# Performance work log

Measured on AMD Instinct MI355X. Metric: run time of the kernel, lower is better.

Reference implementation:

```python
import jax, jax.numpy as jnp
import numpy as np

D_MODEL, NUM_HEADS, D_HEAD, N_CTX = 768, 12, 64, 2048
BATCH = 2


def setup_inputs() -> dict:
    key = jax.random.key(0)
    kx, kk, kq, kv, ko = jax.random.split(key, 5)
    s = 1.0 / np.sqrt(D_MODEL).astype(np.float32)
    x = jax.random.normal(kx, (BATCH, N_CTX, D_MODEL), dtype=jnp.float32)
    W_K = jax.random.normal(kk, (NUM_HEADS, D_HEAD, D_MODEL), dtype=jnp.float32) * s
    W_Q = jax.random.normal(kq, (NUM_HEADS, D_HEAD, D_MODEL), dtype=jnp.float32) * s
    W_V = jax.random.normal(kv, (NUM_HEADS, D_HEAD, D_MODEL), dtype=jnp.float32) * s
    W_O = jax.random.normal(ko, (D_MODEL, D_HEAD * NUM_HEADS), dtype=jnp.float32) * s
    return {"x": x, "W_K": W_K, "W_Q": W_Q, "W_V": W_V, "W_O": W_O}


def reference(x, W_K, W_Q, W_V, W_O):
    B, P, _ = x.shape
    d_head = W_K.shape[1]
    # per-head projections: [B, H, P, d_head]
    q = jnp.einsum('hed,bpd->bhpe', W_Q, x)
    k = jnp.einsum('hed,bpd->bhpe', W_K, x)
    v = jnp.einsum('hed,bpd->bhpe', W_V, x)
    # causal scores [B, H, Q, K]
    scores = jnp.einsum('bhqe,bhke->bhqk', q, k) / np.sqrt(d_head).astype(np.float32)
    mask = jnp.tril(jnp.ones((P, P), dtype=bool))
    scores = jnp.where(mask, scores, jnp.asarray(-1e9, scores.dtype))
    attn = jax.nn.softmax(scores, axis=-1)
    z = jnp.einsum('bhqk,bhke->bhqe', attn, v)
    # flatten heads head-major: 'b h q e -> b q (h e)'
    z_flat = z.transpose(0, 2, 1, 3).reshape(B, P, -1)
    return jnp.einsum('bpf,df->bpd', z_flat, W_O)
```

## Files before the change

kernel.cpp:

```cpp
#include <hip/hip_runtime.h>
#include <hip/hip_bf16.h>

typedef __attribute__((ext_vector_type(8))) short bf16x8;
typedef __attribute__((ext_vector_type(4))) float f32x4;
typedef __attribute__((ext_vector_type(16))) float f32x16;

static __device__ __forceinline__ unsigned short f2bf(float f) {
  union { float f; unsigned int u; } v; v.f = f;
  unsigned int u = v.u;
  return (unsigned short)((u + 0x7FFFu + ((u >> 16) & 1u)) >> 16);
}

__device__ __forceinline__ void async_ld16(const void* g, void* l) {
  __builtin_amdgcn_global_load_lds(
      (const __attribute__((address_space(1))) unsigned int*)g,
      (__attribute__((address_space(3))) unsigned int*)l, 16, 0, 0);
}

__global__ __launch_bounds__(256) void cvt_all(
    const float* __restrict__ x, const float* __restrict__ wk,
    const float* __restrict__ wq, const float* __restrict__ wv,
    const float* __restrict__ wo,
    unsigned short* __restrict__ x_bf, unsigned short* __restrict__ wkqv4,
    unsigned short* __restrict__ wo4) {
  int i = blockIdx.x * 256 + threadIdx.x;
  int e0 = i * 4;
  if (e0 < 3145728) {
    float4 v = *(const float4*)(x + e0);
    ushort4 r;
    r.x = f2bf(v.x); r.y = f2bf(v.y); r.z = f2bf(v.z); r.w = f2bf(v.w);
    *(ushort4*)(x_bf + e0) = r;
    return;
  }
  int j = e0 - 3145728;
  int a = j / 589824;
  int off = j - a * 589824;
  int nl = off / 768;
  int k = off - nl * 768;
  const float* src;
  unsigned short* dst;
  int m;
  float scale = 1.0f;
  if (a == 0)      { src = wk; m = nl;        dst = wkqv4; }
  else if (a == 1) { src = wq; m = 768 + nl;  dst = wkqv4; scale = 0.18033688011112042f; }
  else if (a == 2) { src = wv; m = 1536 + nl; dst = wkqv4; }
  else             { src = wo; m = nl;        dst = wo4; }
  float4 v = *(const float4*)(src + off);
  long idx = ((long)(m >> 4) * 24 + (k >> 5)) * 512 + (m & 15) * 32 + (k & 31);
  ushort4 r;
  r.x = f2bf(v.x * scale); r.y = f2bf(v.y * scale);
  r.z = f2bf(v.z * scale); r.w = f2bf(v.w * scale);
  *(ushort4*)(dst + idx) = r;
}

template <int MODE>
__device__ __forceinline__ void gemm_body(
    const unsigned short* __restrict__ A,
    const unsigned short* __restrict__ B4,
    void* __restrict__ outK, void* __restrict__ outQ, void* __restrict__ outV,
    int m0, int n0,
    unsigned short (*As)[8192]) {
  const int tid = threadIdx.x;
  const int w = tid >> 6;
  const int l = tid & 63;
  const int g = l >> 4;
  const int c = l & 15;
  const int wr = w >> 1, wc = w & 1;

  f32x4 acc[4][3];
#pragma unroll
  for (int i = 0; i < 4; i++)
#pragma unroll
    for (int j = 0; j < 3; j++) acc[i][j] = (f32x4){0.f, 0.f, 0.f, 0.f};

  const int lrow = l >> 3;
  const int lcolx = ((l & 7) ^ lrow) * 8;
  const unsigned short* pB = B4 + (long)((n0 >> 4) + wc * 3) * 12288 + c * 32 + g * 8;

  auto stageA = [&](int buf, int kt) {
    const int k0 = kt * 64;
#pragma unroll
    for (int cc = 0; cc < 4; ++cc) {
      int chunk = cc * 4 + w;
      int row = chunk * 8 + lrow;
      async_ld16(A + (long)(m0 + row) * 768 + k0 + lcolx, &As[buf][chunk * 512]);
    }
  };
  auto loadB = [&](bf16x8 (*b)[3], int kt) {
#pragma unroll
    for (int ks = 0; ks < 2; ++ks)
#pragma unroll
      for (int ni = 0; ni < 3; ++ni)
        b[ks][ni] = *(const bf16x8*)(pB + (long)ni * 12288 + (kt * 2 + ks) * 512);
  };
  auto step = [&](const bf16x8* asrc, const bf16x8 (*b)[3]) {
  };

  bf16x8 b0[2][3], b1[2][3];
  stageA(0, 0);
  loadB(b0, 0);

#pragma unroll
  for (int kt = 0; kt < 12; kt += 2) {
    if (kt + 1 < 12) loadB(b1, kt + 1);
    __builtin_amdgcn_sched_barrier(0);
    asm volatile("s_waitcnt vmcnt(6)" ::: "memory");
    __builtin_amdgcn_sched_barrier(0);
    __builtin_amdgcn_s_barrier();
    __builtin_amdgcn_sched_barrier(0);
    if (kt + 1 < 12) stageA(1, kt + 1);
#pragma unroll
    for (int ks = 0; ks < 2; ++ks) {
      bf16x8 a[4];
#pragma unroll
      for (int mi = 0; mi < 4; ++mi) {
        int row = wr * 64 + mi * 16 + c;
        int col = (ks * 32 + g * 8) ^ ((row & 7) * 8);
        a[mi] = *(const bf16x8*)&As[0][row * 64 + col];
      }
#pragma unroll
      for (int mi = 0; mi < 4; ++mi)
#pragma unroll
        for (int ni = 0; ni < 3; ++ni)
          acc[mi][ni] = __builtin_amdgcn_mfma_f32_16x16x32_bf16(a[mi], b0[ks][ni], acc[mi][ni], 0, 0, 0);
    }
    if (kt + 2 < 12) loadB(b0, kt + 2);
    __builtin_amdgcn_sched_barrier(0);
    if (kt + 2 < 12) {
      asm volatile("s_waitcnt vmcnt(6)" ::: "memory");
    } else {
      asm volatile("s_waitcnt vmcnt(0)" ::: "memory");
    }
    __builtin_amdgcn_sched_barrier(0);
    __builtin_amdgcn_s_barrier();
    __builtin_amdgcn_sched_barrier(0);
    if (kt + 2 < 12) stageA(0, kt + 2);
#pragma unroll
    for (int ks = 0; ks < 2; ++ks) {
      bf16x8 a[4];
#pragma unroll
      for (int mi = 0; mi < 4; ++mi) {
        int row = wr * 64 + mi * 16 + c;
        int col = (ks * 32 + g * 8) ^ ((row & 7) * 8);
        a[mi] = *(const bf16x8*)&As[1][row * 64 + col];
      }
#pragma unroll
      for (int mi = 0; mi < 4; ++mi)
#pragma unroll
        for (int ni = 0; ni < 3; ++ni)
          acc[mi][ni] = __builtin_amdgcn_mfma_f32_16x16x32_bf16(a[mi], b1[ks][ni], acc[mi][ni], 0, 0, 0);
    }
  }

  if (MODE == 1) {
    float* O = (float*)outK;
#pragma unroll
    for (int mi = 0; mi < 4; ++mi)
#pragma unroll
      for (int ni = 0; ni < 3; ++ni)
#pragma unroll
        for (int r = 0; r < 4; ++r) {
          int m = m0 + wr * 64 + mi * 16 + g * 4 + r;
          int n = n0 + wc * 48 + ni * 16 + c;
          O[(long)m * 768 + n] = acc[mi][ni][r];
        }
  } else {
    const int which = (n0 >= 1536) ? 2 : (n0 >= 768 ? 1 : 0);
    const int nb = n0 - which * 768;
    const int b = m0 >> 11;
    if (which == 2) {
#pragma unroll
      for (int mi = 0; mi < 4; ++mi)
#pragma unroll
        for (int ni = 0; ni < 3; ++ni) {
          int e = nb + wc * 48 + ni * 16 + c;
          int h = e >> 6, el = e & 63;
          long bh = b * 12 + h;
          int p0 = (m0 & 2047) + wr * 64 + mi * 16 + g * 4;
          long idx = bh * 131072 + (p0 >> 4) * 1024 + el * 16 + (p0 & 15);
          ushort4 pk;
          pk.x = f2bf(acc[mi][ni][0]); pk.y = f2bf(acc[mi][ni][1]);
          pk.z = f2bf(acc[mi][ni][2]); pk.w = f2bf(acc[mi][ni][3]);
          *(ushort4*)&((unsigned short*)outV)[idx] = pk;
        }
    } else {
#pragma unroll
      for (int mi = 0; mi < 4; ++mi)
#pragma unroll
        for (int ni = 0; ni < 3; ++ni)
#pragma unroll
          for (int r = 0; r < 4; ++r) {
            int m = m0 + wr * 64 + mi * 16 + g * 4 + r;
            int nn = nb + wc * 48 + ni * 16 + c;
            int p = m & 2047;
            int h = nn >> 6, e = nn & 63;
            unsigned short val = f2bf(acc[mi][ni][r]);
            long bh = b * 12 + h;
            if (which == 0) {
              long idx = bh * 131072 + (p >> 5) * 2048 + (e >> 4) * 512 + (p & 31) * 16 + (e & 15);
              ((unsigned short*)outK)[idx] = val;
            } else {
              ((unsigned short*)outQ)[((bh * 2048 + p) << 6) + e] = val;
            }
          }
    }
  }
}

__global__ __launch_bounds__(256) void gemm_qkv(
    const unsigned short* __restrict__ A,
    const unsigned short* __restrict__ Wkqv4,
    unsigned short* __restrict__ k4b, unsigned short* __restrict__ qb,
    unsigned short* __restrict__ v4b) {
  __shared__ __align__(16) unsigned short As[2][8192];
  const int lb = blockIdx.x;
  const int xcd = lb & 7, idx = lb >> 3;
  const int mg = xcd >> 1, ng = xcd & 1;
  const int mi = idx / 12, ni = idx - 12 * mi;
  gemm_body<0>(A, Wkqv4, k4b, qb, v4b, (mg * 8 + mi) * 128, (ng * 12 + ni) * 96, As);
}

__global__ __launch_bounds__(256) void gemm_out(
    const unsigned short* __restrict__ A,
    const unsigned short* __restrict__ Wo4,
    float* __restrict__ out) {
  __shared__ __align__(16) unsigned short As[2][8192];
  const int lb = blockIdx.x;
  const int xcd = lb & 7, idx = lb >> 3;
  const int mi = idx >> 3, ni = idx & 7;
  gemm_body<1>(A, Wo4, out, nullptr, nullptr, (xcd * 4 + mi) * 128, ni * 96, As);
}

__global__ __launch_bounds__(256) void attn(
    const unsigned short* __restrict__ Q,
    const unsigned short* __restrict__ K4,
    const unsigned short* __restrict__ V4,
    unsigned short* __restrict__ Z) {
  __shared__ float2 Opart[3][16][64];
  __shared__ float Lpart[3][32];
  __shared__ float Linv[32];
  const int bx = blockIdx.x;
  const int cidx = bx / 24;
  const int bh = bx - cidx * 24;
  const int c = 63 - cidx;
  const int tid = threadIdx.x;
  const int w = tid >> 6;
  const int l = tid & 63;
  const int ql = l & 31;
  const int hi = l >> 5;
  const int b = bh / 12, hd = bh - b * 12;
  const long base = (long)bh * 2048 * 64;
  const int q0 = c * 32;

  bf16x8 qf[4];
  {
    const unsigned short* qp = Q + base + (long)(q0 + ql) * 64 + hi * 8;
#pragma unroll
    for (int d = 0; d < 4; ++d) qf[d] = *(const bf16x8*)(qp + d * 16);
  }

  f32x16 o0, o1;
#pragma unroll
  for (int r = 0; r < 16; ++r) { o0[r] = 0.f; o1[r] = 0.f; }
  float lsum = 0.f;

  const unsigned short* kp = K4 + (long)bh * 131072 + ql * 16 + hi * 8;
  const unsigned short* vp = V4 + (long)bh * 131072 + ql * 16 + hi * 8;

  auto loadsub = [&](bf16x8* kf, bf16x8* v0, bf16x8* v1, int s) {
    const unsigned short* kps = kp + (long)s * 2048;
#pragma unroll
    for (int d = 0; d < 4; ++d) kf[d] = *(const bf16x8*)(kps + d * 512);
    const unsigned short* vps = vp + (long)s * 2048;
    v0[0] = *(const bf16x8*)(vps);
    v0[1] = *(const bf16x8*)(vps + 1024);
    v1[0] = *(const bf16x8*)(vps + 512);
    v1[1] = *(const bf16x8*)(vps + 1536);
  };

  auto compute = [&](const bf16x8* kf, const bf16x8* v0, const bf16x8* v1, bool diag) {
    __builtin_amdgcn_s_setprio(1);
    f32x16 s_;
#pragma unroll
    for (int r = 0; r < 16; ++r) s_[r] = 0.f;
#pragma unroll
    for (int d = 0; d < 4; ++d)
      s_ = __builtin_amdgcn_mfma_f32_32x32x16_bf16(kf[d], qf[d], s_, 0, 0, 0);
    __builtin_amdgcn_s_setprio(0);
    if (diag) {
#pragma unroll
      for (int r = 0; r < 16; ++r) {
        int krow = (r & 3) + 8 * (r >> 2) + 4 * hi;
        s_[r] = (krow <= ql) ? s_[r] : -1e30f;
      }
    }
    float p[16];
#pragma unroll
    for (int r = 0; r < 16; ++r) { p[r] = exp2f(s_[r]); lsum += p[r]; }
    unsigned int wpk[8];
#pragma unroll
    for (int i = 0; i < 8; ++i)
      asm("v_cvt_pk_bf16_f32 %0, %1, %2" : "=v"(wpk[i]) : "v"(p[2 * i]), "v"(p[2 * i + 1]));
    asm volatile("v_permlane32_swap_b32 %0, %1" : "+v"(wpk[0]), "+v"(wpk[2]));
    asm volatile("v_permlane32_swap_b32 %0, %1" : "+v"(wpk[1]), "+v"(wpk[3]));
    asm volatile("v_permlane32_swap_b32 %0, %1" : "+v"(wpk[4]), "+v"(wpk[6]));
    asm volatile("v_permlane32_swap_b32 %0, %1" : "+v"(wpk[5]), "+v"(wpk[7]));
    union { unsigned int u[4]; bf16x8 v; } f0, f1;
    f0.u[0] = wpk[0]; f0.u[1] = wpk[1]; f0.u[2] = wpk[2]; f0.u[3] = wpk[3];
    f1.u[0] = wpk[4]; f1.u[1] = wpk[5]; f1.u[2] = wpk[6]; f1.u[3] = wpk[7];
    __builtin_amdgcn_s_setprio(1);
    o0 = __builtin_amdgcn_mfma_f32_32x32x16_bf16(f0.v, v0[0], o0, 0, 0, 0);
    o1 = __builtin_amdgcn_mfma_f32_32x32x16_bf16(f0.v, v1[0], o1, 0, 0, 0);
    o0 = __builtin_amdgcn_mfma_f32_32x32x16_bf16(f1.v, v0[1], o0, 0, 0, 0);
    o1 = __builtin_amdgcn_mfma_f32_32x32x16_bf16(f1.v, v1[1], o1, 0, 0, 0);
    __builtin_amdgcn_s_setprio(0);
  };

  int s = w;
  if (s <= c) {
    bf16x8 kfA[4], vA0[2], vA1[2], kfB[4], vB0[2], vB1[2];
    loadsub(kfA, vA0, vA1, s);
    while (s + 8 <= c) {
      loadsub(kfB, vB0, vB1, s + 4);
      compute(kfA, vA0, vA1, false);
      loadsub(kfA, vA0, vA1, s + 8);
      compute(kfB, vB0, vB1, false);
      s += 8;
    }
    if (s + 4 <= c) {
      loadsub(kfB, vB0, vB1, s + 4);
      compute(kfA, vA0, vA1, false);
      compute(kfB, vB0, vB1, (s + 4) == c);
    } else {
      compute(kfA, vA0, vA1, s == c);
    }
  }

  lsum += __shfl_xor(lsum, 32);

  if (w) {
#pragma unroll
    for (int r = 0; r < 16; ++r) Opart[w - 1][r][l] = make_float2(o0[r], o1[r]);
    if (l < 32) Lpart[w - 1][l] = lsum;
  }
  __syncthreads();
  if (w == 0) {
    float ltot = lsum + Lpart[0][ql] + Lpart[1][ql] + Lpart[2][ql];
    if (l < 32) Linv[l] = 1.0f / ltot;
#pragma unroll
    for (int r = 0; r < 16; ++r) {
      float2 t0 = Opart[0][r][l], t1 = Opart[1][r][l], t2 = Opart[2][r][l];
      o0[r] += t0.x + t1.x + t2.x;
      o1[r] += t0.y + t1.y + t2.y;
    }
#pragma unroll
    for (int r = 0; r < 16; ++r) {
      int qr = (r & 3) + 8 * (r >> 2) + 4 * hi;
      float li = Linv[qr];
      unsigned short* zp = Z + ((long)(b * 2048 + q0 + qr) * 768 + hd * 64 + ql);
      zp[0]  = f2bf(o0[r] * li);
      zp[32] = f2bf(o1[r] * li);
    }
  }
}

extern "C" void kernel_launch(void* const* d_in, const int* in_sizes, int n_in,
                              void* d_out, int out_size, void* d_ws, size_t ws_size,
                              hipStream_t stream) {
  const float* x  = (const float*)d_in[0];
  const float* wk = (const float*)d_in[1];
  const float* wq = (const float*)d_in[2];
  const float* wv = (const float*)d_in[3];
  const float* wo = (const float*)d_in[4];

  unsigned short* ws = (unsigned short*)d_ws;
  unsigned short* x_bf  = ws;
  unsigned short* wkqv4 = x_bf + 3145728;
  unsigned short* wo4   = wkqv4 + 1769472;
  unsigned short* qb    = wo4 + 589824;
  unsigned short* k4b   = qb + 3145728;
  unsigned short* v4b   = k4b + 3145728;
  unsigned short* zb    = v4b + 3145728;

  cvt_all<<<5376, 256, 0, stream>>>(x, wk, wq, wv, wo, x_bf, wkqv4, wo4);
  gemm_qkv<<<768, 256, 0, stream>>>(x_bf, wkqv4, k4b, qb, v4b);
  attn<<<1536, 256, 0, stream>>>(qb, k4b, v4b, zb);
  gemm_out<<<256, 256, 0, stream>>>(zb, wo4, (float*)d_out);
}
```

Before: 79.36 us.

## Process two adjacent query chunks per attention block to reuse K/V loads

Each attention block now handles two consecutive 32-row query chunks, so each K/V sub-tile loaded from global memory feeds both chunks' score and PV MFMAs. The grid is halved and launch bounds request two blocks per SM. This cuts K/V load traffic per query, in exchange for more registers (two accumulator sets, two Q fragments), double the LDS for the reduction, and possibly lower occupancy or worse load balance across the causal triangle.

New measurement: 75.87 us. 4.4% less time.

```diff
diff --git a/kernel.cpp b/kernel.cpp
--- a/kernel.cpp
+++ b/kernel.cpp
@@ -93,8 +93,6 @@
       for (int ni = 0; ni < 3; ++ni)
         b[ks][ni] = *(const bf16x8*)(pB + (long)ni * 12288 + (kt * 2 + ks) * 512);
   };
-  auto step = [&](const bf16x8* asrc, const bf16x8 (*b)[3]) {
-  };
 
   bf16x8 b0[2][3], b1[2][3];
   stageA(0, 0);
@@ -231,18 +229,19 @@
   gemm_body<1>(A, Wo4, out, nullptr, nullptr, (xcd * 4 + mi) * 128, ni * 96, As);
 }
 
-__global__ __launch_bounds__(256) void attn(
+__global__ __launch_bounds__(256, 2) void attn(
     const unsigned short* __restrict__ Q,
     const unsigned short* __restrict__ K4,
     const unsigned short* __restrict__ V4,
     unsigned short* __restrict__ Z) {
-  __shared__ float2 Opart[3][16][64];
-  __shared__ float Lpart[3][32];
-  __shared__ float Linv[32];
+  __shared__ float2 Opart[3][2][16][64];
+  __shared__ float Lpart[3][2][32];
+  __shared__ float Linv[2][32];
   const int bx = blockIdx.x;
   const int cidx = bx / 24;
   const int bh = bx - cidx * 24;
-  const int c = 63 - cidx;
+  const int pp = 31 - cidx;
+  const int c0 = 2 * pp, c1 = 2 * pp + 1;
   const int tid = threadIdx.x;
   const int w = tid >> 6;
   const int l = tid & 63;
@@ -250,19 +249,22 @@
   const int hi = l >> 5;
   const int b = bh / 12, hd = bh - b * 12;
   const long base = (long)bh * 2048 * 64;
-  const int q0 = c * 32;
-
-  bf16x8 qf[4];
+
+  bf16x8 qf0[4], qf1[4];
   {
-    const unsigned short* qp = Q + base + (long)(q0 + ql) * 64 + hi * 8;
-#pragma unroll
-    for (int d = 0; d < 4; ++d) qf[d] = *(const bf16x8*)(qp + d * 16);
-  }
-
-  f32x16 o0, o1;
-#pragma unroll
-  for (int r = 0; r < 16; ++r) { o0[r] = 0.f; o1[r] = 0.f; }
-  float lsum = 0.f;
+    const unsigned short* qp0 = Q + base + (long)(c0 * 32 + ql) * 64 + hi * 8;
+    const unsigned short* qp1 = Q + base + (long)(c1 * 32 + ql) * 64 + hi * 8;
+#pragma unroll
+    for (int d = 0; d < 4; ++d) {
+      qf0[d] = *(const bf16x8*)(qp0 + d * 16);
+      qf1[d] = *(const bf16x8*)(qp1 + d * 16);
+    }
+  }
+
+  f32x16 oA0, oA1, oB0, oB1;
+#pragma unroll
+  for (int r = 0; r < 16; ++r) { oA0[r] = 0.f; oA1[r] = 0.f; oB0[r] = 0.f; oB1[r] = 0.f; }
+  float ls0 = 0.f, ls1 = 0.f;
 
   const unsigned short* kp = K4 + (long)bh * 131072 + ql * 16 + hi * 8;
   const unsigned short* vp = V4 + (long)bh * 131072 + ql * 16 + hi * 8;
@@ -278,7 +280,9 @@
     v1[1] = *(const bf16x8*)(vps + 1536);
   };
 
-  auto compute = [&](const bf16x8* kf, const bf16x8* v0, const bf16x8* v1, bool diag) {
+  auto compute_one = [&](const bf16x8* kf, const bf16x8* v0, const bf16x8* v1,
+                         const bf16x8* qf, f32x16& o0, f32x16& o1, float& lsum,
+                         bool diag) {
     __builtin_amdgcn_s_setprio(1);
     f32x16 s_;
 #pragma unroll
@@ -316,50 +320,67 @@
     __builtin_amdgcn_s_setprio(0);
   };
 
+  auto comp_pair = [&](const bf16x8* kf, const bf16x8* v0, const bf16x8* v1, int s) {
+    compute_one(kf, v0, v1, qf1, oB0, oB1, ls1, s == c1);
+    if (s <= c0) compute_one(kf, v0, v1, qf0, oA0, oA1, ls0, s == c0);
+  };
+
   int s = w;
-  if (s <= c) {
+  if (s <= c1) {
     bf16x8 kfA[4], vA0[2], vA1[2], kfB[4], vB0[2], vB1[2];
     loadsub(kfA, vA0, vA1, s);
-    while (s + 8 <= c) {
+    while (s + 8 <= c1) {
       loadsub(kfB, vB0, vB1, s + 4);
-      compute(kfA, vA0, vA1, false);
+      comp_pair(kfA, vA0, vA1, s);
       loadsub(kfA, vA0, vA1, s + 8);
-      compute(kfB, vB0, vB1, false);
+      comp_pair(kfB, vB0, vB1, s + 4);
       s += 8;
     }
-    if (s + 4 <= c) {
+    if (s + 4 <= c1) {
       loadsub(kfB, vB0, vB1, s + 4);
-      compute(kfA, vA0, vA1, false);
-      compute(kfB, vB0, vB1, (s + 4) == c);
+      comp_pair(kfA, vA0, vA1, s);
+      comp_pair(kfB, vB0, vB1, s + 4);
     } else {
-      compute(kfA, vA0, vA1, s == c);
-    }
-  }
-
-  lsum += __shfl_xor(lsum, 32);
+      comp_pair(kfA, vA0, vA1, s);
+    }
+  }
+
+  ls0 += __shfl_xor(ls0, 32);
+  ls1 += __shfl_xor(ls1, 32);
 
   if (w) {
 #pragma unroll
-    for (int r = 0; r < 16; ++r) Opart[w - 1][r][l] = make_float2(o0[r], o1[r]);
-    if (l < 32) Lpart[w - 1][l] = lsum;
+    for (int r = 0; r < 16; ++r) {
+      Opart[w - 1][0][r][l] = make_float2(oA0[r], oA1[r]);
+      Opart[w - 1][1][r][l] = make_float2(oB0[r], oB1[r]);
+    }
+    if (l < 32) { Lpart[w - 1][0][l] = ls0; Lpart[w - 1][1][l] = ls1; }
   }
   __syncthreads();
   if (w == 0) {
-    float ltot = lsum + Lpart[0][ql] + Lpart[1][ql] + Lpart[2][ql];
-    if (l < 32) Linv[l] = 1.0f / ltot;
+    float lt0 = ls0 + Lpart[0][0][ql] + Lpart[1][0][ql] + Lpart[2][0][ql];
+    float lt1 = ls1 + Lpart[0][1][ql] + Lpart[1][1][ql] + Lpart[2][1][ql];
+    if (l < 32) { Linv[0][l] = 1.0f / lt0; Linv[1][l] = 1.0f / lt1; }
 #pragma unroll
     for (int r = 0; r < 16; ++r) {
-      float2 t0 = Opart[0][r][l], t1 = Opart[1][r][l], t2 = Opart[2][r][l];
-      o0[r] += t0.x + t1.x + t2.x;
-      o1[r] += t0.y + t1.y + t2.y;
+      float2 t0 = Opart[0][0][r][l], t1 = Opart[1][0][r][l], t2 = Opart[2][0][r][l];
+      oA0[r] += t0.x + t1.x + t2.x;
+      oA1[r] += t0.y + t1.y + t2.y;
+      float2 u0 = Opart[0][1][r][l], u1 = Opart[1][1][r][l], u2 = Opart[2][1][r][l];
+      oB0[r] += u0.x + u1.x + u2.x;
+      oB1[r] += u0.y + u1.y + u2.y;
     }
 #pragma unroll
     for (int r = 0; r < 16; ++r) {
       int qr = (r & 3) + 8 * (r >> 2) + 4 * hi;
-      float li = Linv[qr];
-      unsigned short* zp = Z + ((long)(b * 2048 + q0 + qr) * 768 + hd * 64 + ql);
-      zp[0]  = f2bf(o0[r] * li);
-      zp[32] = f2bf(o1[r] * li);
+      float li0 = Linv[0][qr];
+      float li1 = Linv[1][qr];
+      unsigned short* zp0 = Z + ((long)(b * 2048 + c0 * 32 + qr) * 768 + hd * 64 + ql);
+      unsigned short* zp1 = Z + ((long)(b * 2048 + c1 * 32 + qr) * 768 + hd * 64 + ql);
+      zp0[0]  = f2bf(oA0[r] * li0);
+      zp0[32] = f2bf(oA1[r] * li0);
+      zp1[0]  = f2bf(oB0[r] * li1);
+      zp1[32] = f2bf(oB1[r] * li1);
     }
   }
 }
@@ -384,6 +405,6 @@
 
   cvt_all<<<5376, 256, 0, stream>>>(x, wk, wq, wv, wo, x_bf, wkqv4, wo4);
   gemm_qkv<<<768, 256, 0, stream>>>(x_bf, wkqv4, k4b, qb, v4b);
-  attn<<<1536, 256, 0, stream>>>(qb, k4b, v4b, zb);
+  attn<<<768, 256, 0, stream>>>(qb, k4b, v4b, zb);
   gemm_out<<<256, 256, 0, stream>>>(zb, wo4, (float*)d_out);
 }
```
